# Kernel optimization log

Hardware: AMD Instinct MI355X
Metric: run time of the kernel (lower is better)

## Reference

```python
import jax, jax.numpy as jnp
import numpy as np

DIM, HEADS = 768, 12


def setup_inputs() -> dict:
    key = jax.random.key(0)
    ks = jax.random.split(key, 9)
    B, N, C, H = 4, 1024, DIM, HEADS
    s = 0.02
    return {
        "x": jax.random.normal(ks[0], (B, N, C), jnp.float32),
        "W_qkv": jax.random.normal(ks[1], (C, 3 * C), jnp.float32) * s,
        "W_proj": jax.random.normal(ks[2], (C, C), jnp.float32) * s,
        "b_proj": jax.random.normal(ks[3], (C,), jnp.float32) * s,
        "W_l": jax.random.normal(ks[4], (H, H), jnp.float32) * s,
        "b_l": jax.random.normal(ks[5], (H,), jnp.float32) * s,
        "W_w": jax.random.normal(ks[6], (H, H), jnp.float32) * s,
        "b_w": jax.random.normal(ks[7], (H,), jnp.float32) * s,
        "lamb": jax.random.normal(ks[8], (H,), jnp.float32) * 0.1,
    }


def reference(x, W_qkv, W_proj, b_proj, W_l, b_l, W_w, b_w, lamb):
    B, N, C = x.shape
    H = W_l.shape[0]
    d = C // H
    scale = d ** -0.5

    qkv = (x @ W_qkv).reshape(B, N, 3, H, d)  # [B,N,3,H,d]
    q = qkv[:, :, 0].transpose(0, 2, 1, 3) * scale  # [B,H,N,d]
    k = qkv[:, :, 1].transpose(0, 2, 1, 3)
    v = qkv[:, :, 2].transpose(0, 2, 1, 3)

    attn = jnp.einsum("bhnd,bhmd->bhnm", q, k)  # [B,H,N,N]
    # talking-heads mix before softmax (proj_l over head axis)
    attn = jnp.einsum("bhnm,hg->bgnm", attn, W_l) + b_l[None, :, None, None]
    attn = jax.nn.softmax(attn, axis=-1)
    # talking-heads mix after softmax (proj_w)
    attn = jnp.einsum("bhnm,hg->bgnm", attn, W_w) + b_w[None, :, None, None]

    # attnscale reaction term: (h-1)*(attn - I)@attn + attn, h=4
    eye = jnp.eye(N, dtype=attn.dtype)
    reaction = 3.0 * jnp.einsum("bhnk,bhkm->bhnm", attn - eye, attn) + attn
    attn = attn + lamb[None, :, None, None] * reaction

    out = jnp.einsum("bhnm,bhmd->bhnd", attn, v)  # [B,H,N,d]
    out = out.transpose(0, 2, 1, 3).reshape(B, N, C)
    return out @ W_proj + b_proj
```

## Files before the change

### kernel.cpp

```cpp
#include <hip/hip_runtime.h>
#include <hip/hip_bf16.h>
#include <stdint.h>

#define B_ 4
#define N_ 1024
#define C_ 768
#define H_ 12
#define D_ 64

typedef unsigned short u16;
typedef __attribute__((ext_vector_type(8))) short bf16x8;
typedef __attribute__((ext_vector_type(4))) float f32x4;

#define AS1 __attribute__((address_space(1)))
#define AS3 __attribute__((address_space(3)))

__device__ __forceinline__ u16 f2b(float f) {
    union { float f; uint32_t u; } x; x.f = f;
    uint32_t r = x.u + 0x7fffu + ((x.u >> 16) & 1u);
    return (u16)(r >> 16);
}
__device__ __forceinline__ float b2f(u16 b) {
    union { uint32_t u; float f; } x; x.u = ((uint32_t)b) << 16;
    return x.f;
}
__device__ __forceinline__ uint32_t cvtpk(float lo, float hi) {
    uint32_t r;
    asm("v_cvt_pk_bf16_f32 %0, %1, %2" : "=v"(r) : "v"(lo), "v"(hi));
    return r;
}

__device__ __forceinline__ void gload16(const void* g, void* lds) {
    __builtin_amdgcn_global_load_lds((const AS1 uint32_t*)g, (AS3 uint32_t*)lds, 16, 0, 0);
}

__device__ __forceinline__ void stage_tile(const u16* __restrict__ g, int ld,
                                           u16* lds, int rows, int w, int l) {
    int nchunk = rows >> 3;
    for (int j = w; j < nchunk; j += 4) {
        int base = j << 10;
        int lanebyte = base + (l << 4);
        int row  = lanebyte >> 7;
        int slot = ((lanebyte >> 4) & 7) ^ (row & 7);
        const u16* src = g + row * ld + (slot << 3);
        gload16(src, (char*)lds + base);
    }
}

__device__ __forceinline__ bf16x8 frag_ld(const u16* lds, int row, int k) {
    int byte = (row << 7) + (k << 1);
    byte ^= (row & 7) << 4;
    return *(const bf16x8*)((const char*)lds + byte);
}

__device__ __forceinline__ f32x4 mfma_bf16(bf16x8 a, bf16x8 b, f32x4 c) {
    return __builtin_amdgcn_mfma_f32_16x16x32_bf16(a, b, c, 0, 0, 0);
}


__global__ void k_cvt(const float* __restrict__ in, u16* __restrict__ outb) {
    int i = blockIdx.x * blockDim.x + threadIdx.x;
    float4 v = ((const float4*)in)[i];
    ushort4 o;
    o.x = f2b(v.x); o.y = f2b(v.y); o.z = f2b(v.z); o.w = f2b(v.w);
    ((ushort4*)outb)[i] = o;
}

__global__ void k_transcvt(const float* __restrict__ in, u16* __restrict__ outb,
                           int R, int Cc) {
    __shared__ float t[32][33];
    int bc = blockIdx.x * 32, br = blockIdx.y * 32;
    int tid = threadIdx.x;
    for (int i = 0; i < 4; i++) {
        int idx = i * 256 + tid; int r = idx >> 5, c = idx & 31;
        t[r][c] = in[(size_t)(br + r) * Cc + bc + c];
    }
    __syncthreads();
    for (int i = 0; i < 4; i++) {
        int idx = i * 256 + tid; int c = idx >> 5, r = idx & 31;
        outb[(size_t)(bc + c) * R + br + r] = f2b(t[r][c]);
    }
}

__global__ void k_vT(const u16* __restrict__ qkv, u16* __restrict__ vT) {
    __shared__ u16 t[64][72];
    int blk = blockIdx.x;
    int nt = blk & 15, h = (blk >> 4) % H_, b = blk / (H_ * 16);
    int tid = threadIdx.x;
    const u16* src = qkv + ((size_t)(b * N_ + nt * 64)) * (3 * C_) + 2 * C_ + h * 64;
    for (int i = 0; i < 16; i++) {
        int idx = i * 256 + tid; int n = idx >> 6, dd = idx & 63;
        t[n][dd] = src[(size_t)n * (3 * C_) + dd];
    }
    __syncthreads();
    u16* dst = vT + ((size_t)(b * H_ + h) * D_) * N_ + nt * 64;
    for (int i = 0; i < 16; i++) {
        int idx = i * 256 + tid; int dd = idx >> 6, n = idx & 63;
        dst[(size_t)dd * N_ + n] = t[n][dd];
    }
}


__global__ __launch_bounds__(256, 2)
void k_gemm_qkv(const u16* __restrict__ xb, const u16* __restrict__ WT,
                u16* __restrict__ qkv) {
    __shared__ __attribute__((aligned(128))) u16 As[128 * 64];
    __shared__ __attribute__((aligned(128))) u16 Bs[128 * 64];
    int tid = threadIdx.x, w = tid >> 6, l = tid & 63;
    int row0 = blockIdx.x * 128, col0 = blockIdx.y * 128;
    f32x4 acc[4][4] = {};
    int wr = (w >> 1) * 64, wc = (w & 1) * 64;
    int fr = l & 15, fq = l >> 4;
    for (int k0 = 0; k0 < C_; k0 += 64) {
        stage_tile(xb + (size_t)row0 * C_ + k0, C_, As, 128, w, l);
        stage_tile(WT + (size_t)col0 * C_ + k0, C_, Bs, 128, w, l);
        __syncthreads();
        #pragma unroll
        for (int kk = 0; kk < 64; kk += 32) {
            bf16x8 af[4], bfr[4];
            #pragma unroll
            for (int i = 0; i < 4; i++) af[i] = frag_ld(As, wr + i * 16 + fr, kk + fq * 8);
            #pragma unroll
            for (int j = 0; j < 4; j++) bfr[j] = frag_ld(Bs, wc + j * 16 + fr, kk + fq * 8);
            #pragma unroll
            for (int i = 0; i < 4; i++)
                #pragma unroll
                for (int j = 0; j < 4; j++)
                    acc[i][j] = mfma_bf16(af[i], bfr[j], acc[i][j]);
        }
        __syncthreads();
    }
    #pragma unroll
    for (int i = 0; i < 4; i++) {
        #pragma unroll
        for (int j = 0; j < 4; j++) {
            int col = col0 + wc + j * 16 + fr;
            float s = (col < C_) ? 0.125f : 1.0f;
            #pragma unroll
            for (int r = 0; r < 4; r++) {
                int row = row0 + wr + i * 16 + fq * 4 + r;
                qkv[(size_t)row * (3 * C_) + col] = f2b(acc[i][j][r] * s);
            }
        }
    }
}


__global__ __launch_bounds__(256, 2)
void k_gemm_qk(const u16* __restrict__ qkv, u16* __restrict__ S) {
    __shared__ __attribute__((aligned(128))) u16 pool[128 * 132];
    u16* As = pool;
    u16* Bs = pool + 128 * 64;
    int tid = threadIdx.x, w = tid >> 6, l = tid & 63;
    int blk = blockIdx.x;
    int bh = blk >> 6, t = blk & 63;
    int b = bh / H_, h = bh % H_;
    int tm = t >> 3, tn = t & 7;
    const u16* qbase = qkv + (size_t)(b * N_) * (3 * C_) + h * 64;
    const u16* kbase = qkv + (size_t)(b * N_) * (3 * C_) + C_ + h * 64;
    f32x4 acc[4][4] = {};
    int wr = (w >> 1) * 64, wc = (w & 1) * 64;
    int fr = l & 15, fq = l >> 4;
    stage_tile(qbase + (size_t)(tm * 128) * (3 * C_), 3 * C_, As, 128, w, l);
    stage_tile(kbase + (size_t)(tn * 128) * (3 * C_), 3 * C_, Bs, 128, w, l);
    __syncthreads();
    #pragma unroll
    for (int kk = 0; kk < 64; kk += 32) {
        bf16x8 af[4], bfr[4];
        #pragma unroll
        for (int i = 0; i < 4; i++) af[i] = frag_ld(As, wr + i * 16 + fr, kk + fq * 8);
        #pragma unroll
        for (int j = 0; j < 4; j++) bfr[j] = frag_ld(Bs, wc + j * 16 + fr, kk + fq * 8);
        #pragma unroll
        for (int i = 0; i < 4; i++)
            #pragma unroll
            for (int j = 0; j < 4; j++)
                acc[i][j] = mfma_bf16(af[i], bfr[j], acc[i][j]);
    }
    __syncthreads();
    u16* Cs = pool;
    #pragma unroll
    for (int i = 0; i < 4; i++) {
        #pragma unroll
        for (int j = 0; j < 4; j++) {
            int lcol = wc + j * 16 + fr;
            #pragma unroll
            for (int r = 0; r < 4; r++) {
                int lrow = wr + i * 16 + fq * 4 + r;
                Cs[lrow * 132 + lcol] = f2b(acc[i][j][r]);
            }
        }
    }
    __syncthreads();
    for (int q = 0; q < 16; q++) {
        int idx = q * 256 + tid;
        int lrow = idx >> 5, lc = idx & 31;
        ushort4 v = *(const ushort4*)&Cs[lrow * 132 + lc * 4];
        *(ushort4*)(S + ((size_t)(b * N_ + tm * 128 + lrow) * H_ + h) * N_
                      + tn * 128 + lc * 4) = v;
    }
}


__global__ __launch_bounds__(256)
void k_mix_softmax(const u16* __restrict__ S, u16* __restrict__ Pw,
                   const float* __restrict__ Wl, const float* __restrict__ Ww,
                   const float* __restrict__ bw) {
    __shared__ __attribute__((aligned(16))) u16 Sb[4][2][256][8];
    __shared__ float Zl[4][16];
    __shared__ float sWl[144], sWw[144], sbw16[16];
    int tid = threadIdx.x;
    int wv = tid >> 6, l = tid & 63;
    int m_l = l & 15, gr = l >> 4;
    if (tid < 144) { sWl[tid] = Wl[tid]; sWw[tid] = Ww[tid]; }
    if (tid < 16) sbw16[tid] = (tid < 12) ? bw[tid] : 0.f;
    __syncthreads();

    int blk = blockIdx.x;
    int b = blk >> 10, n = blk & 1023;
    const u16* srow = S + ((size_t)(b * N_ + n) * H_) * N_ + wv * 256;

    for (int p = 0; p < 4; p++) {
        int m = p * 64 + l;
        #pragma unroll
        for (int hb = 0; hb < 2; hb++) {
            bf16x8 pk;
            #pragma unroll
            for (int j = 0; j < 8; j++) {
                int h = hb * 8 + j;
                ((u16*)&pk)[j] = (h < 12) ? srow[(size_t)h * N_ + m] : (u16)0;
            }
            *(bf16x8*)&Sb[wv][hb][m][0] = pk;
        }
    }

    bf16x8 a1;
    #pragma unroll
    for (int j = 0; j < 8; j++) {
        int h = gr * 8 + j;
        int ok = (m_l < 12) & (h < 12);
        int idx = ok ? (h * 12 + m_l) : 0;
        float wval = ok ? sWl[idx] : 0.f;
        ((u16*)&a1)[j] = f2b(wval);
    }

    float z0 = 0.f, z1 = 0.f, z2 = 0.f, z3 = 0.f;
    uint32_t E0[16], E1[16];
    #pragma unroll
    for (int grp = 0; grp < 16; grp++) {
        bf16x8 bs = {};
        if (gr < 2) bs = *(const bf16x8*)&Sb[wv][gr][grp * 16 + m_l][0];
        f32x4 c = {0.f, 0.f, 0.f, 0.f};
        c = mfma_bf16(a1, bs, c);
        float e0 = __expf(c[0]), e1 = __expf(c[1]);
        float e2 = __expf(c[2]), e3 = __expf(c[3]);
        z0 += e0; z1 += e1; z2 += e2; z3 += e3;
        E0[grp] = cvtpk(e0, e1);
        E1[grp] = cvtpk(e2, e3);
    }

    #pragma unroll
    for (int off = 1; off < 16; off <<= 1) {
        z0 += __shfl_xor(z0, off);
        z1 += __shfl_xor(z1, off);
        z2 += __shfl_xor(z2, off);
        z3 += __shfl_xor(z3, off);
    }
    if (m_l == 0) {
        Zl[wv][gr * 4 + 0] = z0; Zl[wv][gr * 4 + 1] = z1;
        Zl[wv][gr * 4 + 2] = z2; Zl[wv][gr * 4 + 3] = z3;
    }
    __syncthreads();

    bf16x8 a2;
    #pragma unroll
    for (int j = 0; j < 8; j++) {
        int h = gr * 8 + j;
        float v = 0.f;
        if ((m_l < 12) & (h < 12)) {
            float zz = Zl[0][h] + Zl[1][h] + Zl[2][h] + Zl[3][h];
            v = sWw[h * 12 + m_l] / zz;
        }
        ((u16*)&a2)[j] = f2b(v);
    }

    f32x4 cb;
    cb[0] = sbw16[gr * 4 + 0]; cb[1] = sbw16[gr * 4 + 1];
    cb[2] = sbw16[gr * 4 + 2]; cb[3] = sbw16[gr * 4 + 3];
    int la = m_l + (((2 * gr) & 3) << 4);
    int lb = m_l + (((2 * gr + 1) & 3) << 4);
    u16* Pb = (u16*)&Sb[wv][0][0][0];
    #pragma unroll
    for (int grp = 0; grp < 16; grp++) {
        union { int4 i4; bf16x8 v; } u;
        u.i4.x = __shfl((int)E0[grp], la);
        u.i4.y = __shfl((int)E1[grp], la);
        u.i4.z = __shfl((int)E0[grp], lb);
        u.i4.w = __shfl((int)E1[grp], lb);
        f32x4 c = cb;
        c = mfma_bf16(a2, u.v, c);
        if (gr < 3) {
            uint32_t w01 = cvtpk(c[0], c[1]);
            uint32_t w23 = cvtpk(c[2], c[3]);
            int g0 = gr * 4, mm = grp * 16 + m_l;
            Pb[(g0 + 0) * 276 + mm] = (u16)w01;
            Pb[(g0 + 1) * 276 + mm] = (u16)(w01 >> 16);
            Pb[(g0 + 2) * 276 + mm] = (u16)w23;
            Pb[(g0 + 3) * 276 + mm] = (u16)(w23 >> 16);
        }
    }

    for (int g = 0; g < 12; g++) {
        ushort4 v = *(const ushort4*)&Pb[g * 276 + l * 4];
        *(ushort4*)(Pw + ((size_t)(b * H_ + g) * N_ + n) * N_ + wv * 256 + l * 4) = v;
    }
}


template <int MODE>
__global__ __launch_bounds__(256, 2)
void k_gemm_av(const u16* __restrict__ Pw, const u16* __restrict__ BT,
               u16* __restrict__ outp, const u16* __restrict__ qkv,
               const float* __restrict__ lamb) {
    __shared__ __attribute__((aligned(128))) u16 As[128 * 64];
    __shared__ __attribute__((aligned(128))) u16 Bs[64 * 64];
    int tid = threadIdx.x, w = tid >> 6, l = tid & 63;
    int blk = blockIdx.x;
    int bh = blk >> 3, tm = blk & 7;
    int b = bh / H_, h = bh % H_;
    const u16* Abase = Pw + ((size_t)bh * N_ + tm * 128) * N_;
    const u16* Bbase = BT + (size_t)bh * D_ * N_;
    f32x4 acc[2][4] = {};
    int wrow = w * 32;
    int fr = l & 15, fq = l >> 4;
    for (int k0 = 0; k0 < N_; k0 += 64) {
        stage_tile(Abase + k0, N_, As, 128, w, l);
        stage_tile(Bbase + k0, N_, Bs, 64, w, l);
        __syncthreads();
        #pragma unroll
        for (int kk = 0; kk < 64; kk += 32) {
            bf16x8 af[2], bfr[4];
            #pragma unroll
            for (int i = 0; i < 2; i++) af[i] = frag_ld(As, wrow + i * 16 + fr, kk + fq * 8);
            #pragma unroll
            for (int j = 0; j < 4; j++) bfr[j] = frag_ld(Bs, j * 16 + fr, kk + fq * 8);
            #pragma unroll
            for (int i = 0; i < 2; i++)
                #pragma unroll
                for (int j = 0; j < 4; j++)
                    acc[i][j] = mfma_bf16(af[i], bfr[j], acc[i][j]);
        }
        __syncthreads();
    }
    float lam = (MODE == 0) ? lamb[h] : 0.f;
    #pragma unroll
    for (int i = 0; i < 2; i++) {
        #pragma unroll
        for (int j = 0; j < 4; j++) {
            int col = j * 16 + fr;
            int rowb = tm * 128 + wrow + i * 16 + fq * 4;
            if (MODE == 0) {
                ushort4 zo;
                #pragma unroll
                for (int r = 0; r < 4; r++) {
                    float vv = b2f(qkv[(size_t)(b * N_ + rowb + r) * (3 * C_) + 2 * C_ + h * 64 + col]);
                    float zv = (1.f - 2.f * lam) * vv + 3.f * lam * acc[i][j][r];
                    ((u16*)&zo)[r] = f2b(zv);
                }
                *(ushort4*)(outp + ((size_t)bh * D_ + col) * N_ + rowb) = zo;
            } else {
                #pragma unroll
                for (int r = 0; r < 4; r++)
                    outp[(size_t)(b * N_ + rowb + r) * C_ + h * 64 + col] = f2b(acc[i][j][r]);
            }
        }
    }
}


__global__ __launch_bounds__(256, 2)
void k_gemm_proj(const u16* __restrict__ o, const u16* __restrict__ WT,
                 const float* __restrict__ bias, float* __restrict__ out) {
    __shared__ __attribute__((aligned(128))) u16 As[128 * 64];
    __shared__ __attribute__((aligned(128))) u16 Bs[128 * 64];
    int tid = threadIdx.x, w = tid >> 6, l = tid & 63;
    int row0 = blockIdx.x * 128, col0 = blockIdx.y * 128;
    f32x4 acc[4][4] = {};
    int wr = (w >> 1) * 64, wc = (w & 1) * 64;
    int fr = l & 15, fq = l >> 4;
    for (int k0 = 0; k0 < C_; k0 += 64) {
        stage_tile(o + (size_t)row0 * C_ + k0, C_, As, 128, w, l);
        stage_tile(WT + (size_t)col0 * C_ + k0, C_, Bs, 128, w, l);
        __syncthreads();
        #pragma unroll
        for (int kk = 0; kk < 64; kk += 32) {
            bf16x8 af[4], bfr[4];
            #pragma unroll
            for (int i = 0; i < 4; i++) af[i] = frag_ld(As, wr + i * 16 + fr, kk + fq * 8);
            #pragma unroll
            for (int j = 0; j < 4; j++) bfr[j] = frag_ld(Bs, wc + j * 16 + fr, kk + fq * 8);
            #pragma unroll
            for (int i = 0; i < 4; i++)
                #pragma unroll
                for (int j = 0; j < 4; j++)
                    acc[i][j] = mfma_bf16(af[i], bfr[j], acc[i][j]);
        }
        __syncthreads();
    }
    #pragma unroll
    for (int i = 0; i < 4; i++) {
        #pragma unroll
        for (int j = 0; j < 4; j++) {
            int col = col0 + wc + j * 16 + fr;
            float bv = bias[col];
            #pragma unroll
            for (int r = 0; r < 4; r++) {
                int row = row0 + wr + i * 16 + fq * 4 + r;
                out[(size_t)row * C_ + col] = acc[i][j][r] + bv;
            }
        }
    }
}


extern "C" void kernel_launch(void* const* d_in, const int* in_sizes, int n_in,
                              void* d_out, int out_size, void* d_ws, size_t ws_size,
                              hipStream_t stream) {
    const float* x     = (const float*)d_in[0];
    const float* Wqkv  = (const float*)d_in[1];
    const float* Wproj = (const float*)d_in[2];
    const float* bproj = (const float*)d_in[3];
    const float* Wl    = (const float*)d_in[4];
    const float* Ww    = (const float*)d_in[6];
    const float* bw    = (const float*)d_in[7];
    const float* lamb  = (const float*)d_in[8];
    float* out = (float*)d_out;
    char* ws = (char*)d_ws;

    constexpr size_t SZ_S   = (size_t)B_ * N_ * H_ * N_ * 2;
    constexpr size_t SZ_QKV = (size_t)B_ * N_ * 3 * C_ * 2;
    constexpr size_t SZ_U   = (size_t)B_ * H_ * N_ * D_ * 2;
    constexpr size_t SZ_XB  = (size_t)B_ * N_ * C_ * 2;
    constexpr size_t SZ_WQT = (size_t)C_ * 3 * C_ * 2;

    u16* S      = (u16*)(ws);
    u16* zT     = (u16*)(ws);
    u16* o      = (u16*)(ws + SZ_U);
    u16* Pw     = (u16*)(ws + SZ_S);
    u16* qkv    = (u16*)(ws + 2 * SZ_S);
    u16* xb     = (u16*)(ws + 2 * SZ_S + SZ_QKV);
    u16* vT     = xb;
    u16* WqkvT  = (u16*)(ws + 2 * SZ_S + SZ_QKV + SZ_XB);
    u16* WprojT = (u16*)(ws + 2 * SZ_S + SZ_QKV + SZ_XB + SZ_WQT);

    k_cvt<<<3072, 256, 0, stream>>>(x, xb);
    k_transcvt<<<dim3(72, 24), 256, 0, stream>>>(Wqkv, WqkvT, C_, 3 * C_);
    k_transcvt<<<dim3(24, 24), 256, 0, stream>>>(Wproj, WprojT, C_, C_);
    k_gemm_qkv<<<dim3(32, 18), 256, 0, stream>>>(xb, WqkvT, qkv);
    k_vT<<<B_ * H_ * 16, 256, 0, stream>>>(qkv, vT);
    k_gemm_qk<<<B_ * H_ * 64, 256, 0, stream>>>(qkv, S);
    k_mix_softmax<<<B_ * N_, 256, 0, stream>>>(S, Pw, Wl, Ww, bw);
    k_gemm_av<0><<<B_ * H_ * 8, 256, 0, stream>>>(Pw, vT, zT, qkv, lamb);
    k_gemm_av<1><<<B_ * H_ * 8, 256, 0, stream>>>(Pw, zT, o, nullptr, nullptr);
    k_gemm_proj<<<dim3(32, 6), 256, 0, stream>>>(o, WprojT, bproj, out);
}
```

Measured before the change: 178.6 us.

## Software-pipeline S loads in mix_softmax, shrink LDS, reuse vT in AV epilogue

The mix-softmax kernel now loads S in four 64-column chunks into registers and double-buffers them in a smaller LDS array, so the next chunk's global loads overlap the current chunk's MFMA and exp work. Output staging is also done per chunk with a smaller padded stride, which cuts LDS use and may raise occupancy. The QK epilogue padding changes from 132 to 130, and the AV mode-0 epilogue reads v from the transposed vT buffer as a vector load instead of doing strided scalar reads from qkv. Per-chunk writes to Pw are smaller and could coalesce less well.

```diff
diff --git a/kernel.cpp b/kernel.cpp
--- a/kernel.cpp
+++ b/kernel.cpp
@@ -187,7 +187,7 @@
             #pragma unroll
             for (int r = 0; r < 4; r++) {
                 int lrow = wr + i * 16 + fq * 4 + r;
-                Cs[lrow * 132 + lcol] = f2b(acc[i][j][r]);
+                Cs[lrow * 130 + lcol] = f2b(acc[i][j][r]);
             }
         }
     }
@@ -195,7 +195,7 @@
     for (int q = 0; q < 16; q++) {
         int idx = q * 256 + tid;
         int lrow = idx >> 5, lc = idx & 31;
-        ushort4 v = *(const ushort4*)&Cs[lrow * 132 + lc * 4];
+        ushort4 v = *(const ushort4*)&Cs[lrow * 130 + lc * 4];
         *(ushort4*)(S + ((size_t)(b * N_ + tm * 128 + lrow) * H_ + h) * N_
                       + tn * 128 + lc * 4) = v;
     }
@@ -206,7 +206,7 @@
 void k_mix_softmax(const u16* __restrict__ S, u16* __restrict__ Pw,
                    const float* __restrict__ Wl, const float* __restrict__ Ww,
                    const float* __restrict__ bw) {
-    __shared__ __attribute__((aligned(16))) u16 Sb[4][2][256][8];
+    __shared__ __attribute__((aligned(16))) u16 Sb[4][2][2][64][8];
     __shared__ float Zl[4][16];
     __shared__ float sWl[144], sWw[144], sbw16[16];
     int tid = threadIdx.x;
@@ -220,20 +220,6 @@
     int b = blk >> 10, n = blk & 1023;
     const u16* srow = S + ((size_t)(b * N_ + n) * H_) * N_ + wv * 256;
 
-    for (int p = 0; p < 4; p++) {
-        int m = p * 64 + l;
-        #pragma unroll
-        for (int hb = 0; hb < 2; hb++) {
-            bf16x8 pk;
-            #pragma unroll
-            for (int j = 0; j < 8; j++) {
-                int h = hb * 8 + j;
-                ((u16*)&pk)[j] = (h < 12) ? srow[(size_t)h * N_ + m] : (u16)0;
-            }
-            *(bf16x8*)&Sb[wv][hb][m][0] = pk;
-        }
-    }
-
     bf16x8 a1;
     #pragma unroll
     for (int j = 0; j < 8; j++) {
@@ -244,19 +230,38 @@
         ((u16*)&a1)[j] = f2b(wval);
     }
 
+    u16 pf[12];
+    #pragma unroll
+    for (int h = 0; h < 12; h++) pf[h] = srow[(size_t)h * N_ + l];
+
     float z0 = 0.f, z1 = 0.f, z2 = 0.f, z3 = 0.f;
     uint32_t E0[16], E1[16];
     #pragma unroll
-    for (int grp = 0; grp < 16; grp++) {
-        bf16x8 bs = {};
-        if (gr < 2) bs = *(const bf16x8*)&Sb[wv][gr][grp * 16 + m_l][0];
-        f32x4 c = {0.f, 0.f, 0.f, 0.f};
-        c = mfma_bf16(a1, bs, c);
-        float e0 = __expf(c[0]), e1 = __expf(c[1]);
-        float e2 = __expf(c[2]), e3 = __expf(c[3]);
-        z0 += e0; z1 += e1; z2 += e2; z3 += e3;
-        E0[grp] = cvtpk(e0, e1);
-        E1[grp] = cvtpk(e2, e3);
+    for (int ch = 0; ch < 4; ch++) {
+        bf16x8 p0, p1 = {};
+        #pragma unroll
+        for (int j = 0; j < 8; j++) ((u16*)&p0)[j] = pf[j];
+        #pragma unroll
+        for (int j = 0; j < 4; j++) ((u16*)&p1)[j] = pf[8 + j];
+        *(bf16x8*)&Sb[wv][ch & 1][0][l][0] = p0;
+        *(bf16x8*)&Sb[wv][ch & 1][1][l][0] = p1;
+        if (ch < 3) {
+            #pragma unroll
+            for (int h = 0; h < 12; h++)
+                pf[h] = srow[(size_t)h * N_ + (ch + 1) * 64 + l];
+        }
+        #pragma unroll
+        for (int grp = 0; grp < 4; grp++) {
+            bf16x8 bs = {};
+            if (gr < 2) bs = *(const bf16x8*)&Sb[wv][ch & 1][gr][grp * 16 + m_l][0];
+            f32x4 c = {0.f, 0.f, 0.f, 0.f};
+            c = mfma_bf16(a1, bs, c);
+            float e0 = __expf(c[0]), e1 = __expf(c[1]);
+            float e2 = __expf(c[2]), e3 = __expf(c[3]);
+            z0 += e0; z1 += e1; z2 += e2; z3 += e3;
+            E0[ch * 4 + grp] = cvtpk(e0, e1);
+            E1[ch * 4 + grp] = cvtpk(e2, e3);
+        }
     }
 
     #pragma unroll
@@ -289,30 +294,36 @@
     cb[2] = sbw16[gr * 4 + 2]; cb[3] = sbw16[gr * 4 + 3];
     int la = m_l + (((2 * gr) & 3) << 4);
     int lb = m_l + (((2 * gr + 1) & 3) << 4);
-    u16* Pb = (u16*)&Sb[wv][0][0][0];
-    #pragma unroll
-    for (int grp = 0; grp < 16; grp++) {
-        union { int4 i4; bf16x8 v; } u;
-        u.i4.x = __shfl((int)E0[grp], la);
-        u.i4.y = __shfl((int)E1[grp], la);
-        u.i4.z = __shfl((int)E0[grp], lb);
-        u.i4.w = __shfl((int)E1[grp], lb);
-        f32x4 c = cb;
-        c = mfma_bf16(a2, u.v, c);
-        if (gr < 3) {
-            uint32_t w01 = cvtpk(c[0], c[1]);
-            uint32_t w23 = cvtpk(c[2], c[3]);
-            int g0 = gr * 4, mm = grp * 16 + m_l;
-            Pb[(g0 + 0) * 276 + mm] = (u16)w01;
-            Pb[(g0 + 1) * 276 + mm] = (u16)(w01 >> 16);
-            Pb[(g0 + 2) * 276 + mm] = (u16)w23;
-            Pb[(g0 + 3) * 276 + mm] = (u16)(w23 >> 16);
-        }
-    }
-
-    for (int g = 0; g < 12; g++) {
-        ushort4 v = *(const ushort4*)&Pb[g * 276 + l * 4];
-        *(ushort4*)(Pw + ((size_t)(b * H_ + g) * N_ + n) * N_ + wv * 256 + l * 4) = v;
+    u16* Pb = (u16*)&Sb[wv][0][0][0][0];
+    #pragma unroll
+    for (int ch = 0; ch < 4; ch++) {
+        #pragma unroll
+        for (int grp = 0; grp < 4; grp++) {
+            int idx = ch * 4 + grp;
+            union { int4 i4; bf16x8 v; } u;
+            u.i4.x = __shfl((int)E0[idx], la);
+            u.i4.y = __shfl((int)E1[idx], la);
+            u.i4.z = __shfl((int)E0[idx], lb);
+            u.i4.w = __shfl((int)E1[idx], lb);
+            f32x4 c = cb;
+            c = mfma_bf16(a2, u.v, c);
+            if (gr < 3) {
+                uint32_t w01 = cvtpk(c[0], c[1]);
+                uint32_t w23 = cvtpk(c[2], c[3]);
+                int g0 = gr * 4, mm = grp * 16 + m_l;
+                Pb[(g0 + 0) * 66 + mm] = (u16)w01;
+                Pb[(g0 + 1) * 66 + mm] = (u16)(w01 >> 16);
+                Pb[(g0 + 2) * 66 + mm] = (u16)w23;
+                Pb[(g0 + 3) * 66 + mm] = (u16)(w23 >> 16);
+            }
+        }
+        #pragma unroll
+        for (int p = 0; p < 3; p++) {
+            int row = p * 4 + gr;
+            ushort4 v = *(const ushort4*)&Pb[row * 66 + m_l * 4];
+            *(ushort4*)(Pw + ((size_t)(b * H_ + row) * N_ + n) * N_
+                          + wv * 256 + ch * 64 + m_l * 4) = v;
+        }
     }
 }
 
@@ -320,8 +331,7 @@
 template <int MODE>
 __global__ __launch_bounds__(256, 2)
 void k_gemm_av(const u16* __restrict__ Pw, const u16* __restrict__ BT,
-               u16* __restrict__ outp, const u16* __restrict__ qkv,
-               const float* __restrict__ lamb) {
+               u16* __restrict__ outp, const float* __restrict__ lamb) {
     __shared__ __attribute__((aligned(128))) u16 As[128 * 64];
     __shared__ __attribute__((aligned(128))) u16 Bs[64 * 64];
     int tid = threadIdx.x, w = tid >> 6, l = tid & 63;
@@ -360,11 +370,12 @@
             int col = j * 16 + fr;
             int rowb = tm * 128 + wrow + i * 16 + fq * 4;
             if (MODE == 0) {
+                ushort4 vv = *(const ushort4*)(BT + ((size_t)bh * D_ + col) * N_ + rowb);
                 ushort4 zo;
                 #pragma unroll
                 for (int r = 0; r < 4; r++) {
-                    float vv = b2f(qkv[(size_t)(b * N_ + rowb + r) * (3 * C_) + 2 * C_ + h * 64 + col]);
-                    float zv = (1.f - 2.f * lam) * vv + 3.f * lam * acc[i][j][r];
+                    float zv = (1.f - 2.f * lam) * b2f(((const u16*)&vv)[r])
+                             + 3.f * lam * acc[i][j][r];
                     ((u16*)&zo)[r] = f2b(zv);
                 }
                 *(ushort4*)(outp + ((size_t)bh * D_ + col) * N_ + rowb) = zo;
@@ -460,7 +471,7 @@
     k_vT<<<B_ * H_ * 16, 256, 0, stream>>>(qkv, vT);
     k_gemm_qk<<<B_ * H_ * 64, 256, 0, stream>>>(qkv, S);
     k_mix_softmax<<<B_ * N_, 256, 0, stream>>>(S, Pw, Wl, Ww, bw);
-    k_gemm_av<0><<<B_ * H_ * 8, 256, 0, stream>>>(Pw, vT, zT, qkv, lamb);
-    k_gemm_av<1><<<B_ * H_ * 8, 256, 0, stream>>>(Pw, zT, o, nullptr, nullptr);
+    k_gemm_av<0><<<B_ * H_ * 8, 256, 0, stream>>>(Pw, vT, zT, lamb);
+    k_gemm_av<1><<<B_ * H_ * 8, 256, 0, stream>>>(Pw, zT, o, nullptr);
     k_gemm_proj<<<dim3(32, 6), 256, 0, stream>>>(o, WprojT, bproj, out);
 }
```

Result: slower. 191.5 us (+7.2%).
